# Optimization experiments

Hardware: AMD Instinct MI355X
Metric: run time of the kernel (lower is better)

Reference implementation:

```python
import jax, jax.numpy as jnp
import numpy as np

B, A = 65536, 32          # batch, n_agents
D, H1, H2, L = 4, 32, 32, 16  # local MLP dims
G_IN, G_H, G_OUT = 2 * L, 32, 2  # global MLP dims


def _lin_init(k, fan_in, fan_out):
    kw, kb = jax.random.split(k)
    s = 1.0 / np.sqrt(fan_in)
    W = jax.random.uniform(kw, (fan_in, fan_out), minval=-s, maxval=s, dtype=jnp.float32)
    b = jax.random.uniform(kb, (fan_out,), minval=-s, maxval=s, dtype=jnp.float32)
    return W, b


def setup_inputs() -> dict:
    key = jax.random.key(0)
    ks = jax.random.split(key, 9)
    x = jax.random.uniform(ks[0], (B, A * D), dtype=jnp.float32)
    oW1, ob1 = _lin_init(ks[1], D, H1)
    oW2, ob2 = _lin_init(ks[2], H1, H2)
    oW3, ob3 = _lin_init(ks[3], H2, L)
    sW1, sb1 = _lin_init(ks[4], D, H1)
    sW2, sb2 = _lin_init(ks[5], H1, H2)
    sW3, sb3 = _lin_init(ks[6], H2, L)
    gW1, gb1 = _lin_init(ks[7], G_IN, G_H)
    gW2, gb2 = _lin_init(ks[8], G_H, G_OUT)
    return {
        "joint_state_actions": x,
        "selected_agent_idx": 5,
        "oW1": oW1, "ob1": ob1, "oW2": oW2, "ob2": ob2, "oW3": oW3, "ob3": ob3,
        "sW1": sW1, "sb1": sb1, "sW2": sW2, "sb2": sb2, "sW3": sW3, "sb3": sb3,
        "gW1": gW1, "gb1": gb1, "gW2": gW2, "gb2": gb2,
    }


def _mlp3(x, W1, b1, W2, b2, W3, b3):
    h = jax.nn.relu(x @ W1 + b1)
    h = jax.nn.relu(h @ W2 + b2)
    return jax.nn.relu(h @ W3 + b3)


def reference(joint_state_actions, selected_agent_idx,
              oW1, ob1, oW2, ob2, oW3, ob3,
              sW1, sb1, sW2, sb2, sW3, sb3,
              gW1, gb1, gW2, gb2):
    xa = joint_state_actions.reshape(-1, A, D)  # [B, A, 4]
    # other-agents stack applied to all agents at once, masked sum over non-selected
    other = _mlp3(xa, oW1, ob1, oW2, ob2, oW3, ob3)  # [B, A, 16]
    mask = (jnp.arange(A) != selected_agent_idx).astype(other.dtype)[None, :, None]
    sum_other = jnp.sum(other * mask, axis=1)  # [B, 16]
    sel_in = xa[:, selected_agent_idx]  # [B, 4] (static index)
    sel_out = _mlp3(sel_in, sW1, sb1, sW2, sb2, sW3, sb3)  # [B, 16]
    h = jax.nn.relu(jnp.concatenate([sel_out, sum_other], axis=1) @ gW1 + gb1)
    q = h @ gW2 + gb2  # [B, 2]
    actions = sel_in[:, 3].astype(jnp.int32)[:, None]  # [B, 1]
    return jnp.take_along_axis(q, actions, axis=1)  # [B, 1]
```

## Files before the change

kernel.cpp:

```cpp
#include <hip/hip_runtime.h>
#include <hip/hip_bf16.h>

#define DEV __device__ __forceinline__

typedef __attribute__((ext_vector_type(8)))  __bf16    bf16x8;
typedef __attribute__((ext_vector_type(4)))  int       int4v;
typedef __attribute__((ext_vector_type(2)))  unsigned  uint2v;
typedef __attribute__((ext_vector_type(16))) float     vfloat16;

#if __has_builtin(__builtin_amdgcn_permlane32_swap)
#define HAVE_PLSWAP 1
#endif

DEV int pkbf(float a, float b) {
    __hip_bfloat162 h = __float22bfloat162_rn(make_float2(a, b));
    int r;
    __builtin_memcpy(&r, &h, sizeof(r));
    return r;
}

DEV bf16x8 i4_to_frag(int4v v) { return __builtin_bit_cast(bf16x8, v); }

DEV vfloat16 mfma32(bf16x8 a, bf16x8 b, vfloat16 c) {
    return __builtin_amdgcn_mfma_f32_32x32x16_bf16(a, b, c, 0, 0, 0);
}

DEV bf16x8 xposeB(float c0, float c1, float c2, float c3,
                  float c4, float c5, float c6, float c7, bool h) {
    int R0 = pkbf(fmaxf(c0, 0.f), fmaxf(c1, 0.f));
    int R1 = pkbf(fmaxf(c2, 0.f), fmaxf(c3, 0.f));
    int R2 = pkbf(fmaxf(c4, 0.f), fmaxf(c5, 0.f));
    int R3 = pkbf(fmaxf(c6, 0.f), fmaxf(c7, 0.f));
#ifdef HAVE_PLSWAP
    uint2v p0 = __builtin_amdgcn_permlane32_swap((unsigned)R0, (unsigned)R2, false, false);
    uint2v p1 = __builtin_amdgcn_permlane32_swap((unsigned)R1, (unsigned)R3, false, false);
    int4v v;
    v.x = (int)p0.x; v.y = (int)p1.x; v.z = (int)p0.y; v.w = (int)p1.y;
#else
    int S0 = h ? R0 : R2;
    int S1 = h ? R1 : R3;
    int Y0 = __shfl_xor(S0, 32, 64);
    int Y1 = __shfl_xor(S1, 32, 64);
    int4v v;
    v.x = h ? Y0 : R0;
    v.y = h ? Y1 : R1;
    v.z = h ? R2 : Y0;
    v.w = h ? R3 : Y1;
#endif
    return i4_to_frag(v);
}

DEV bf16x8 make_afrag(const float* __restrict__ W, const float* __restrict__ bias,
                      int ld, int Mact, int K, int koff, int lane) {
    int m = lane & 31;
    int h = lane >> 5;
    int d[4];
#pragma unroll
    for (int i = 0; i < 4; ++i) {
        int k0 = koff + h * 8 + 2 * i;
        int k1 = k0 + 1;
        float w0 = 0.f, w1 = 0.f;
        if (m < Mact) {
            if (k0 < K) w0 = W[k0 * ld + m];
            else if (bias && k0 == K) w0 = bias[m];
            if (k1 < K) w1 = W[k1 * ld + m];
            else if (bias && k1 == K) w1 = bias[m];
        }
        d[i] = pkbf(w0, w1);
    }
    int4v v; v.x = d[0]; v.y = d[1]; v.z = d[2]; v.w = d[3];
    return i4_to_frag(v);
}

DEV vfloat16 bvec32(const float* __restrict__ b, int lane) {
    int h = lane >> 5;
    vfloat16 v;
#pragma unroll
    for (int reg = 0; reg < 16; ++reg)
        v[reg] = b[(reg & 3) + 8 * (reg >> 2) + 4 * h];
    return v;
}
DEV vfloat16 bvec16(const float* __restrict__ b, int lane) {
    int h = lane >> 5;
    vfloat16 v;
#pragma unroll
    for (int reg = 0; reg < 16; ++reg)
        v[reg] = (reg < 8) ? b[(reg & 3) + 8 * (reg >> 2) + 4 * h] : 0.f;
    return v;
}

DEV vfloat16 zero16() {
    vfloat16 z;
#pragma unroll
    for (int i = 0; i < 16; ++i) z[i] = 0.f;
    return z;
}

DEV bf16x8 make_b1h(float4 xa, bool h) {
    int4v v;
    v.x = h ? 0 : pkbf(xa.x, xa.y);
    v.y = h ? 0 : pkbf(xa.z, xa.w);
    v.z = h ? 0 : 0x00003f80;
    v.w = 0;
    return i4_to_frag(v);
}

struct Frags {
    bf16x8 A1, A2lo, A2hi, A3lo, A3hi;
    vfloat16 b2, b3;
};

DEV void load_frags(Frags& F,
                    const float* __restrict__ W1, const float* __restrict__ b1,
                    const float* __restrict__ W2, const float* __restrict__ b2,
                    const float* __restrict__ W3, const float* __restrict__ b3,
                    int lane) {
    F.A1   = make_afrag(W1, b1,      32, 32, 4,  0,  lane);
    F.A2lo = make_afrag(W2, nullptr, 32, 32, 32, 0,  lane);
    F.A2hi = make_afrag(W2, nullptr, 32, 32, 32, 16, lane);
    F.A3lo = make_afrag(W3, nullptr, 16, 16, 32, 0,  lane);
    F.A3hi = make_afrag(W3, nullptr, 16, 16, 32, 16, lane);
    F.b2 = bvec32(b2, lane);
    F.b3 = bvec16(b3, lane);
}

DEV vfloat16 run_mlp3(bf16x8 B1, const Frags& F, bool h) {
    vfloat16 C = mfma32(F.A1, B1, zero16());
    bf16x8 Blo = xposeB(C[0], C[1], C[2], C[3], C[4], C[5], C[6], C[7], h);
    bf16x8 Bhi = xposeB(C[8], C[9], C[10], C[11], C[12], C[13], C[14], C[15], h);
    vfloat16 C2 = mfma32(F.A2lo, Blo, F.b2);
    C2 = mfma32(F.A2hi, Bhi, C2);
    Blo = xposeB(C2[0], C2[1], C2[2], C2[3], C2[4], C2[5], C2[6], C2[7], h);
    Bhi = xposeB(C2[8], C2[9], C2[10], C2[11], C2[12], C2[13], C2[14], C2[15], h);
    vfloat16 C3 = mfma32(F.A3lo, Blo, F.b3);
    C3 = mfma32(F.A3hi, Bhi, C3);
    return C3;
}

#define XSTRIDE 132

__global__ __launch_bounds__(256, 4)
void dqn_kernel(const float* __restrict__ x, const int* __restrict__ selp,
                const float* __restrict__ oW1, const float* __restrict__ ob1,
                const float* __restrict__ oW2, const float* __restrict__ ob2,
                const float* __restrict__ oW3, const float* __restrict__ ob3,
                const float* __restrict__ sW1, const float* __restrict__ sb1,
                const float* __restrict__ sW2, const float* __restrict__ sb2,
                const float* __restrict__ sW3, const float* __restrict__ sb3,
                const float* __restrict__ gW1, const float* __restrict__ gb1,
                const float* __restrict__ gW2, const float* __restrict__ gb2,
                float* __restrict__ out)
{
    __shared__ float lds_x[32 * XSTRIDE];
    __shared__ float lds_red[3][8][64];

    const int tid  = threadIdx.x;
    const int lane = tid & 63;
    const int wave = tid >> 6;
    const bool h = lane >= 32;
    const int c = lane & 31;
    const int sel = *selp;
    const int base0 = blockIdx.x * 32;

    {
        const float* xblk = x + (size_t)base0 * 128;
#pragma unroll
        for (int k = 0; k < 4; ++k) {
            int f = tid + 256 * k;
            int row = f >> 5;
            int ag  = f & 31;
            float4 v = *(const float4*)(xblk + (size_t)f * 4);
            *(float4*)&lds_x[ag * XSTRIDE + row * 4] = v;
        }
    }

    Frags Fo;
    load_frags(Fo, oW1, ob1, oW2, ob2, oW3, ob3, lane);

    __syncthreads();

    float sum[8] = {0.f, 0.f, 0.f, 0.f, 0.f, 0.f, 0.f, 0.f};
    const int a0 = wave * 8;

    float4 xa = *(const float4*)&lds_x[a0 * XSTRIDE + c * 4];
#pragma unroll
    for (int a = a0; a < a0 + 8; ++a) {
        int an = (a + 1 < a0 + 8) ? a + 1 : a;
        float4 xn = *(const float4*)&lds_x[an * XSTRIDE + c * 4];
        vfloat16 C3 = run_mlp3(make_b1h(xa, h), Fo, h);
        if (a != sel) {
#pragma unroll
            for (int i = 0; i < 8; ++i) sum[i] += fmaxf(C3[i], 0.f);
        }
        xa = xn;
    }

    if (wave != 0) {
#pragma unroll
        for (int i = 0; i < 8; ++i) lds_red[wave - 1][i][lane] = sum[i];
    }
    __syncthreads();

    if (wave == 0) {
#pragma unroll
        for (int j = 0; j < 3; ++j)
#pragma unroll
            for (int i = 0; i < 8; ++i) sum[i] += lds_red[j][i][lane];

        Frags Fs;
        load_frags(Fs, sW1, sb1, sW2, sb2, sW3, sb3, lane);
        float4 xs = *(const float4*)&lds_x[sel * XSTRIDE + c * 4];
        vfloat16 C3s = run_mlp3(make_b1h(xs, h), Fs, h);

        bf16x8 Ag_lo = make_afrag(gW1, nullptr, 32, 32, 32, 0,  lane);
        bf16x8 Ag_hi = make_afrag(gW1, nullptr, 32, 32, 32, 16, lane);
        vfloat16 gb1v = bvec32(gb1, lane);
        bf16x8 Bg_lo = xposeB(C3s[0], C3s[1], C3s[2], C3s[3],
                              C3s[4], C3s[5], C3s[6], C3s[7], h);
        bf16x8 Bg_hi = xposeB(sum[0], sum[1], sum[2], sum[3],
                              sum[4], sum[5], sum[6], sum[7], h);
        vfloat16 G = mfma32(Ag_lo, Bg_lo, gb1v);
        G = mfma32(Ag_hi, Bg_hi, G);
#pragma unroll
        for (int i = 0; i < 16; ++i) G[i] = fmaxf(G[i], 0.f);

        float q0 = 0.f, q1 = 0.f;
#pragma unroll
        for (int reg = 0; reg < 16; ++reg) {
            int row = (reg & 3) + 8 * (reg >> 2) + (h ? 4 : 0);
            q0 += G[reg] * gW2[row * 2 + 0];
            q1 += G[reg] * gW2[row * 2 + 1];
        }
        q0 += __shfl_xor(q0, 32, 64);
        q1 += __shfl_xor(q1, 32, 64);
        q0 += gb2[0];
        q1 += gb2[1];

        if (!h) {
            int act = (int)xs.w;
            act = act < 0 ? 0 : (act > 1 ? 1 : act);
            out[base0 + c] = act ? q1 : q0;
        }
    }
}

extern "C" void kernel_launch(void* const* d_in, const int* in_sizes, int n_in,
                              void* d_out, int out_size, void* d_ws, size_t ws_size,
                              hipStream_t stream) {
    const float* x   = (const float*)d_in[0];
    const int*   sel = (const int*)d_in[1];
    const float* oW1 = (const float*)d_in[2];
    const float* ob1 = (const float*)d_in[3];
    const float* oW2 = (const float*)d_in[4];
    const float* ob2 = (const float*)d_in[5];
    const float* oW3 = (const float*)d_in[6];
    const float* ob3 = (const float*)d_in[7];
    const float* sW1 = (const float*)d_in[8];
    const float* sb1 = (const float*)d_in[9];
    const float* sW2 = (const float*)d_in[10];
    const float* sb2 = (const float*)d_in[11];
    const float* sW3 = (const float*)d_in[12];
    const float* sb3 = (const float*)d_in[13];
    const float* gW1 = (const float*)d_in[14];
    const float* gb1 = (const float*)d_in[15];
    const float* gW2 = (const float*)d_in[16];
    const float* gb2 = (const float*)d_in[17];
    float* out = (float*)d_out;

    const int B = in_sizes[0] / 128;
    const int blocks = B / 32;
    dqn_kernel<<<blocks, 256, 0, stream>>>(x, sel,
                                           oW1, ob1, oW2, ob2, oW3, ob3,
                                           sW1, sb1, sW2, sb2, sW3, sb3,
                                           gW1, gb1, gW2, gb2, out);
}
```

Before: 136.9 us.

## Prefetch selected/global weights to LDS, software-pipeline layer-1 MFMA, cheaper bf16 pack

Several changes at once. bf16 packing now uses a bias-add plus byte-permute instead of the library conversion. The first-layer MFMA for the next agent is issued before the current agent's remaining layers, so the two overlap. The selected-agent and global MLP weights are staged into LDS cooperatively by all threads, so wave 0 no longer does serial global loads in its tail. The launch-bounds occupancy hint is removed and the half-wave zeroing in the layer-1 B fragment is dropped. The bf16 rounding no longer handles ties-to-even or NaN, and the extra LDS and registers may lower occupancy.

```diff
diff --git a/kernel.cpp b/kernel.cpp
--- a/kernel.cpp
+++ b/kernel.cpp
@@ -13,10 +13,9 @@
 #endif
 
 DEV int pkbf(float a, float b) {
-    __hip_bfloat162 h = __float22bfloat162_rn(make_float2(a, b));
-    int r;
-    __builtin_memcpy(&r, &h, sizeof(r));
-    return r;
+    unsigned ua = __builtin_bit_cast(unsigned, a) + 0x8000u;
+    unsigned ub = __builtin_bit_cast(unsigned, b) + 0x8000u;
+    return (int)__builtin_amdgcn_perm(ua, ub, 0x03020706u);
 }
 
 DEV bf16x8 i4_to_frag(int4v v) { return __builtin_bit_cast(bf16x8, v); }
@@ -96,11 +95,11 @@
     return z;
 }
 
-DEV bf16x8 make_b1h(float4 xa, bool h) {
+DEV bf16x8 make_b1(float4 xa) {
     int4v v;
-    v.x = h ? 0 : pkbf(xa.x, xa.y);
-    v.y = h ? 0 : pkbf(xa.z, xa.w);
-    v.z = h ? 0 : 0x00003f80;
+    v.x = pkbf(xa.x, xa.y);
+    v.y = pkbf(xa.z, xa.w);
+    v.z = 0x00003f80;
     v.w = 0;
     return i4_to_frag(v);
 }
@@ -124,10 +123,9 @@
     F.b3 = bvec16(b3, lane);
 }
 
-DEV vfloat16 run_mlp3(bf16x8 B1, const Frags& F, bool h) {
-    vfloat16 C = mfma32(F.A1, B1, zero16());
-    bf16x8 Blo = xposeB(C[0], C[1], C[2], C[3], C[4], C[5], C[6], C[7], h);
-    bf16x8 Bhi = xposeB(C[8], C[9], C[10], C[11], C[12], C[13], C[14], C[15], h);
+DEV vfloat16 finish_mlp(vfloat16 C1, const Frags& F, bool h) {
+    bf16x8 Blo = xposeB(C1[0], C1[1], C1[2], C1[3], C1[4], C1[5], C1[6], C1[7], h);
+    bf16x8 Bhi = xposeB(C1[8], C1[9], C1[10], C1[11], C1[12], C1[13], C1[14], C1[15], h);
     vfloat16 C2 = mfma32(F.A2lo, Blo, F.b2);
     C2 = mfma32(F.A2hi, Bhi, C2);
     Blo = xposeB(C2[0], C2[1], C2[2], C2[3], C2[4], C2[5], C2[6], C2[7], h);
@@ -139,7 +137,23 @@
 
 #define XSTRIDE 132
 
-__global__ __launch_bounds__(256, 4)
+#define OFF_SW1 0
+#define OFF_SB1 128
+#define OFF_SW2 160
+#define OFF_SB2 1184
+#define OFF_SW3 1216
+#define OFF_SB3 1728
+#define OFF_GW1 1744
+#define OFF_GB1 2768
+#define OFF_GW2 2800
+#define OFF_GB2 2864
+#define WTOT    2866
+
+DEV void cpw(float* __restrict__ dst, const float* __restrict__ src, int n, int tid) {
+    for (int i = tid; i < n; i += 256) dst[i] = src[i];
+}
+
+__global__ __launch_bounds__(256)
 void dqn_kernel(const float* __restrict__ x, const int* __restrict__ selp,
                 const float* __restrict__ oW1, const float* __restrict__ ob1,
                 const float* __restrict__ oW2, const float* __restrict__ ob2,
@@ -153,6 +167,7 @@
 {
     __shared__ float lds_x[32 * XSTRIDE];
     __shared__ float lds_red[3][8][64];
+    __shared__ float lds_w[WTOT];
 
     const int tid  = threadIdx.x;
     const int lane = tid & 63;
@@ -172,6 +187,16 @@
             float4 v = *(const float4*)(xblk + (size_t)f * 4);
             *(float4*)&lds_x[ag * XSTRIDE + row * 4] = v;
         }
+        cpw(lds_w + OFF_SW1, sW1, 128,  tid);
+        cpw(lds_w + OFF_SB1, sb1, 32,   tid);
+        cpw(lds_w + OFF_SW2, sW2, 1024, tid);
+        cpw(lds_w + OFF_SB2, sb2, 32,   tid);
+        cpw(lds_w + OFF_SW3, sW3, 512,  tid);
+        cpw(lds_w + OFF_SB3, sb3, 16,   tid);
+        cpw(lds_w + OFF_GW1, gW1, 1024, tid);
+        cpw(lds_w + OFF_GB1, gb1, 32,   tid);
+        cpw(lds_w + OFF_GW2, gW2, 64,   tid);
+        cpw(lds_w + OFF_GB2, gb2, 2,    tid);
     }
 
     Frags Fo;
@@ -181,18 +206,22 @@
 
     float sum[8] = {0.f, 0.f, 0.f, 0.f, 0.f, 0.f, 0.f, 0.f};
     const int a0 = wave * 8;
-
-    float4 xa = *(const float4*)&lds_x[a0 * XSTRIDE + c * 4];
-#pragma unroll
-    for (int a = a0; a < a0 + 8; ++a) {
-        int an = (a + 1 < a0 + 8) ? a + 1 : a;
-        float4 xn = *(const float4*)&lds_x[an * XSTRIDE + c * 4];
-        vfloat16 C3 = run_mlp3(make_b1h(xa, h), Fo, h);
-        if (a != sel) {
-#pragma unroll
-            for (int i = 0; i < 8; ++i) sum[i] += fmaxf(C3[i], 0.f);
-        }
-        xa = xn;
+    const float* xbase = &lds_x[a0 * XSTRIDE + c * 4];
+
+    vfloat16 C1 = mfma32(Fo.A1, make_b1(*(const float4*)xbase), zero16());
+#pragma unroll
+    for (int i = 0; i < 8; ++i) {
+        vfloat16 C1n;
+        if (i < 7) {
+            float4 xn = *(const float4*)(xbase + (i + 1) * XSTRIDE);
+            C1n = mfma32(Fo.A1, make_b1(xn), zero16());
+        }
+        vfloat16 C3 = finish_mlp(C1, Fo, h);
+        if (a0 + i != sel) {
+#pragma unroll
+            for (int j = 0; j < 8; ++j) sum[j] += fmaxf(C3[j], 0.f);
+        }
+        if (i < 7) C1 = C1n;
     }
 
     if (wave != 0) {
@@ -208,13 +237,16 @@
             for (int i = 0; i < 8; ++i) sum[i] += lds_red[j][i][lane];
 
         Frags Fs;
-        load_frags(Fs, sW1, sb1, sW2, sb2, sW3, sb3, lane);
+        load_frags(Fs, lds_w + OFF_SW1, lds_w + OFF_SB1,
+                       lds_w + OFF_SW2, lds_w + OFF_SB2,
+                       lds_w + OFF_SW3, lds_w + OFF_SB3, lane);
         float4 xs = *(const float4*)&lds_x[sel * XSTRIDE + c * 4];
-        vfloat16 C3s = run_mlp3(make_b1h(xs, h), Fs, h);
-
-        bf16x8 Ag_lo = make_afrag(gW1, nullptr, 32, 32, 32, 0,  lane);
-        bf16x8 Ag_hi = make_afrag(gW1, nullptr, 32, 32, 32, 16, lane);
-        vfloat16 gb1v = bvec32(gb1, lane);
+        vfloat16 C1s = mfma32(Fs.A1, make_b1(xs), zero16());
+        vfloat16 C3s = finish_mlp(C1s, Fs, h);
+
+        bf16x8 Ag_lo = make_afrag(lds_w + OFF_GW1, nullptr, 32, 32, 32, 0,  lane);
+        bf16x8 Ag_hi = make_afrag(lds_w + OFF_GW1, nullptr, 32, 32, 32, 16, lane);
+        vfloat16 gb1v = bvec32(lds_w + OFF_GB1, lane);
         bf16x8 Bg_lo = xposeB(C3s[0], C3s[1], C3s[2], C3s[3],
                               C3s[4], C3s[5], C3s[6], C3s[7], h);
         bf16x8 Bg_hi = xposeB(sum[0], sum[1], sum[2], sum[3],
@@ -224,17 +256,18 @@
 #pragma unroll
         for (int i = 0; i < 16; ++i) G[i] = fmaxf(G[i], 0.f);
 
+        const float* gw2l = lds_w + OFF_GW2;
         float q0 = 0.f, q1 = 0.f;
 #pragma unroll
         for (int reg = 0; reg < 16; ++reg) {
             int row = (reg & 3) + 8 * (reg >> 2) + (h ? 4 : 0);
-            q0 += G[reg] * gW2[row * 2 + 0];
-            q1 += G[reg] * gW2[row * 2 + 1];
+            q0 += G[reg] * gw2l[row * 2 + 0];
+            q1 += G[reg] * gw2l[row * 2 + 1];
         }
         q0 += __shfl_xor(q0, 32, 64);
         q1 += __shfl_xor(q1, 32, 64);
-        q0 += gb2[0];
-        q1 += gb2[1];
+        q0 += lds_w[OFF_GB2 + 0];
+        q1 += lds_w[OFF_GB2 + 1];
 
         if (!h) {
             int act = (int)xs.w;
```

Result: slower. 149.4 us (+9.1%).
